# Performance work log

Measured on AMD Instinct MI355X. Metric: run time of the kernel, lower is better.

The kernel has to match this reference:

```python
import jax, jax.numpy as jnp
import numpy as np

B, N, D = 4, 4096, 1024
H, DH = 16, 64  # heads, dim_head; inner_dim = H*DH = 1024
EPS = 1e-6


def setup_inputs() -> dict:
    key = jax.random.key(0)
    ks = jax.random.split(key, 6)
    s = 1.0 / np.sqrt(D)
    return {
        "x": jax.random.normal(ks[0], (B, N, D), dtype=jnp.float32),
        "Wq": jax.random.normal(ks[1], (D, H * DH), dtype=jnp.float32) * s,
        "Wk": jax.random.normal(ks[2], (D, H * DH), dtype=jnp.float32) * s,
        "Wv": jax.random.normal(ks[3], (D, H * DH), dtype=jnp.float32) * s,
        "Wo": jax.random.normal(ks[4], (H * DH, D), dtype=jnp.float32) * s,
        "bo": jnp.zeros((D,), dtype=jnp.float32),
    }


def reference(x, Wq, Wk, Wv, Wo, bo):
    # projections, split heads: b n (h d) -> b h n d
    def split_heads(t):
        b, n, _ = t.shape
        return t.reshape(b, n, H, DH).transpose(0, 2, 1, 3)

    q = split_heads(x @ Wq)
    k = split_heads(x @ Wk)  # context = x (self-attention)
    v = split_heads(x @ Wv)

    # elu feature map: elu(x) + 1
    q = jax.nn.elu(q) + 1.0
    k = jax.nn.elu(k) + 1.0

    # normalizer z[b,h,n,1] = q . sum_n k  + eps
    k_sum = k.sum(axis=2)                                  # b h d
    z = jnp.einsum('bhnd,bhd->bhn', q, k_sum)[..., None] + EPS

    # kv outer-product reduction: O(N d^2)
    kv = jnp.einsum('bhnd,bhne->bhde', k, v)               # b h d e
    out = jnp.einsum('bhnd,bhde->bhne', q, kv) / z         # b h n e

    # merge heads: b h n d -> b n (h d)
    out = out.transpose(0, 2, 1, 3).reshape(x.shape[0], x.shape[1], H * DH)
    return out @ Wo + bo
```

## Files before the change

kernel.cpp:

```cpp
#include <hip/hip_runtime.h>
#include <hip/hip_bf16.h>


#define DEV_INLINE __device__ __forceinline__

typedef short bf16x8 __attribute__((ext_vector_type(8)));
typedef float f32x4  __attribute__((ext_vector_type(4)));

static constexpr int Bb = 4, Nn = 4096, Dd = 1024, Hh = 16, DHd = 64;
static constexpr int Mrows = Bb * Nn;

DEV_INLINE float bf2f(short s) {
  unsigned u = ((unsigned)(unsigned short)s) << 16;
  float f; __builtin_memcpy(&f, &u, 4); return f;
}
DEV_INLINE short f2bf(float f) {
  unsigned u; __builtin_memcpy(&u, &f, 4);
  unsigned r = (u + 0x7fffu + ((u >> 16) & 1u)) >> 16;
  return (short)r;
}

DEV_INLINE void gload16(const void* g, void* l) {
  typedef __attribute__((address_space(1))) const void gv_t;
  typedef __attribute__((address_space(3))) void lv_t;
  __builtin_amdgcn_global_load_lds((gv_t*)g, (lv_t*)l, 16, 0, 0);
}

DEV_INLINE int lds_off(int r_, int c_) {
  return r_ * 128 + ((((c_ >> 3) ^ (r_ & 7)) << 3) | (c_ & 7));
}


__global__ void convert_x_kernel(const float* __restrict__ x, short* __restrict__ xb) {
  const int total = Mrows * 1024 / 4;
  for (int i = blockIdx.x * 256 + threadIdx.x; i < total; i += 2048 * 256) {
    float4 v = ((const float4*)x)[i];
    short4 o;
    o.x = f2bf(v.x); o.y = f2bf(v.y); o.z = f2bf(v.z); o.w = f2bf(v.w);
    ((short4*)xb)[i] = o;
  }
}

__global__ void transposeW_kernel(const float* __restrict__ Wq, const float* __restrict__ Wk,
                                  const float* __restrict__ Wv, const float* __restrict__ Wo,
                                  short* __restrict__ Wt, short* __restrict__ WoT) {
  int z = blockIdx.z;
  const float* W = (z == 0) ? Wq : (z == 1) ? Wk : (z == 2) ? Wv : Wo;
  short* dstb = (z < 3) ? (Wt + (size_t)z * 1024 * 1024) : WoT;
  __shared__ float tile[64][69];
  int t = threadIdx.x;
  int r = t >> 2, c4 = (t & 3) << 4;
  const float* src = W + (blockIdx.y * 64 + r) * 1024 + blockIdx.x * 64 + c4;
  for (int j = 0; j < 4; ++j) {
    float4 v = ((const float4*)src)[j];
    tile[r][c4 + 4 * j + 0] = v.x;
    tile[r][c4 + 4 * j + 1] = v.y;
    tile[r][c4 + 4 * j + 2] = v.z;
    tile[r][c4 + 4 * j + 3] = v.w;
  }
  __syncthreads();
  __attribute__((aligned(16))) short tmp[16];
  for (int j = 0; j < 16; ++j) tmp[j] = f2bf(tile[c4 + j][r]);
  short* dst = dstb + (blockIdx.x * 64 + r) * 1024 + blockIdx.y * 64 + c4;
  ((int4*)dst)[0] = ((int4*)tmp)[0];
  ((int4*)dst)[1] = ((int4*)tmp)[1];
}

template <int MODE>
__global__ __launch_bounds__(256, 2) void gemm128_kernel(
    const short* __restrict__ A, const short* __restrict__ Bt,
    short* __restrict__ q, short* __restrict__ kT, short* __restrict__ vT,
    float* __restrict__ out, const float* __restrict__ bias, int nTilesN) {
  __shared__ __align__(16) short sm[128 * 128];
  short* smA = sm;
  short* smB = sm + 8192;
  const int K = 1024;
  int bid0 = blockIdx.x;
  int xcd = bid0 & 7, local = bid0 >> 3;
  int chunk = local >> 6, rem = local & 63;
  int ncc = nTilesN >> 3;
  int cm = chunk / ncc, cn = chunk % ncc;
  int tm = xcd * 16 + cm * 8 + (rem >> 3);
  int tn = cn * 8 + (rem & 7);

  int t = threadIdx.x, w = t >> 6, lane = t & 63;
  int rl = lane & 15, kg = lane >> 4;
  int wr = w >> 1, wc = w & 1;
  const short* Abase = A + (size_t)tm * 128 * K;
  const short* Bbase = Bt + (size_t)tn * 128 * K;

  f32x4 acc[4][4] = {};
  for (int k0 = 0; k0 < K; k0 += 64) {
    __syncthreads();
    for (int p = 0; p < 4; ++p) {
      int c = p * 256 + t;
      int row = c >> 3, u = c & 7;
      int off = ((u ^ (row & 7)) << 3);
      gload16(Abase + row * K + k0 + off, (char*)smA + p * 4096 + w * 1024);
      gload16(Bbase + row * K + k0 + off, (char*)smB + p * 4096 + w * 1024);
    }
    __syncthreads();
    for (int kk = 0; kk < 2; ++kk) {
      int slot = kk * 4 + kg;
      bf16x8 af[4], bfr[4];
      for (int mt = 0; mt < 4; ++mt) {
        int row = wr * 64 + mt * 16 + rl;
        af[mt] = *(const bf16x8*)&smA[row * 64 + ((slot ^ (row & 7)) << 3)];
      }
      for (int nt = 0; nt < 4; ++nt) {
        int row = wc * 64 + nt * 16 + rl;
        bfr[nt] = *(const bf16x8*)&smB[row * 64 + ((slot ^ (row & 7)) << 3)];
      }
      for (int mt = 0; mt < 4; ++mt)
        for (int nt = 0; nt < 4; ++nt)
          acc[mt][nt] = __builtin_amdgcn_mfma_f32_16x16x32_bf16(af[mt], bfr[nt], acc[mt][nt], 0, 0, 0);
    }
  }
  if (MODE == 1) {
    float* smf = (float*)sm;
    __syncthreads();
    for (int h = 0; h < 2; ++h) {
      if (wr == h) {
        for (int mt = 0; mt < 4; ++mt)
          for (int nt = 0; nt < 4; ++nt)
            for (int r = 0; r < 4; ++r)
              smf[(mt * 16 + kg * 4 + r) * 128 + wc * 64 + nt * 16 + rl] = acc[mt][nt][r];
      }
      __syncthreads();
      for (int i = 0; i < 8; ++i) {
        int idx = i * 256 + t;
        int row = idx >> 5, c4 = (idx & 31) << 2;
        float4 v = *(const float4*)&smf[row * 128 + c4];
        float4 bv = *(const float4*)&bias[tn * 128 + c4];
        v.x += bv.x; v.y += bv.y; v.z += bv.z; v.w += bv.w;
        *(float4*)&out[(size_t)(tm * 128 + h * 64 + row) * Dd + tn * 128 + c4] = v;
      }
      __syncthreads();
    }
    return;
  }
  __syncthreads();
  int sec = tn >> 3;
  int tloc = tn & 7;
  for (int mt = 0; mt < 4; ++mt)
    for (int nt = 0; nt < 4; ++nt)
      for (int r = 0; r < 4; ++r) {
        float v = acc[mt][nt][r];
        if (sec <= 1) v = v > 0.f ? v + 1.f : __expf(v);
        int row = wr * 64 + mt * 16 + kg * 4 + r;
        int col = wc * 64 + nt * 16 + rl;
        int o = (sec == 0) ? lds_off(row, col) : lds_off(col, row);
        sm[o] = f2bf(v);
      }
  __syncthreads();
  if (sec == 0) {
    for (int i = 0; i < 8; ++i) {
      int idx = i * 256 + t;
      int row = idx >> 4, c = idx & 15;
      int col0 = c * 8;
      int gcol = tloc * 128 + col0;
      int h = gcol >> 6, d0 = gcol & 63;
      int grow = tm * 128 + row;
      int b = grow >> 12, n = grow & 4095;
      *(int4*)&q[(((size_t)(b * Hh + h)) * Nn + n) * DHd + d0] = *(const int4*)&sm[lds_off(row, col0)];
    }
  } else {
    short* dst = (sec == 1) ? kT : vT;
    for (int i = 0; i < 8; ++i) {
      int idx = i * 256 + t;
      int dcol = idx >> 4, c = idx & 15;
      int n0 = c * 8;
      int gcol = tloc * 128 + dcol;
      int h = gcol >> 6, d = gcol & 63;
      int grow0 = tm * 128 + n0;
      int b = grow0 >> 12, n = grow0 & 4095;
      *(int4*)&dst[(((size_t)(b * Hh + h)) * DHd + d) * Nn + n] = *(const int4*)&sm[lds_off(dcol, n0)];
    }
  }
}

__global__ void ksum_kernel(const short* __restrict__ kT, float* __restrict__ ksp) {
  int bh = blockIdx.x >> 3, seg = blockIdx.x & 7;
  int t = threadIdx.x;
  int d = t >> 2, sub = t & 3;
  const short* row = kT + ((size_t)bh * DHd + d) * Nn + seg * 512;
  float s = 0.f;
  for (int i = sub * 8; i < 512; i += 32) {
    bf16x8 v = *(const bf16x8*)&row[i];
    for (int j = 0; j < 8; ++j) s += bf2f(v[j]);
  }
  s += __shfl_xor(s, 1);
  s += __shfl_xor(s, 2);
  if (sub == 0) ksp[(bh * 8 + seg) * 64 + d] = s;
}

__global__ __launch_bounds__(256, 2) void kv_kernel(const short* __restrict__ kT,
                                                    const short* __restrict__ vT,
                                                    float* __restrict__ kvp) {
  __shared__ __align__(16) short smK[64 * 128];
  __shared__ __align__(16) short smV[64 * 128];
  int bh = blockIdx.x, seg = blockIdx.y;
  int t = threadIdx.x;
  int w = t >> 6, lane = t & 63, rl = lane & 15, kg = lane >> 4;
  const short* kb = kT + (size_t)bh * DHd * Nn + seg * 1024;
  const short* vb = vT + (size_t)bh * DHd * Nn + seg * 1024;
  f32x4 acc[4] = {};
  for (int n0 = 0; n0 < 1024; n0 += 128) {
    __syncthreads();
    for (int p = 0; p < 4; ++p) {
      int c = p * 256 + t;
      int row = c >> 4, u = c & 15;
      int off = ((u ^ (row & 15)) << 3);
      gload16(kb + row * Nn + n0 + off, (char*)smK + p * 4096 + w * 1024);
      gload16(vb + row * Nn + n0 + off, (char*)smV + p * 4096 + w * 1024);
    }
    __syncthreads();
    for (int kk = 0; kk < 4; ++kk) {
      int slot = kk * 4 + kg;
      int rowA = w * 16 + rl;
      bf16x8 a = *(const bf16x8*)&smK[rowA * 128 + ((slot ^ (rowA & 15)) << 3)];
      for (int nt = 0; nt < 4; ++nt) {
        int rowB = nt * 16 + rl;
        bf16x8 b = *(const bf16x8*)&smV[rowB * 128 + ((slot ^ (rowB & 15)) << 3)];
        acc[nt] = __builtin_amdgcn_mfma_f32_16x16x32_bf16(a, b, acc[nt], 0, 0, 0);
      }
    }
  }
  float* smf = (float*)smK;
  __syncthreads();
  for (int nt = 0; nt < 4; ++nt)
    for (int r = 0; r < 4; ++r)
      smf[(nt * 16 + rl) * 64 + (w * 16 + kg * 4 + r)] = acc[nt][r];
  __syncthreads();
  float* dst = kvp + ((size_t)(bh * 4 + seg)) * 4096;
  for (int i = 0; i < 4; ++i) {
    int idx = i * 256 + t;
    int e = idx >> 4, c4 = (idx & 15) << 2;
    *(float4*)&dst[e * 64 + c4] = *(const float4*)&smf[e * 64 + c4];
  }
}

__global__ void kvc_kernel(const float* __restrict__ kvp, short* __restrict__ kvT) {
  int bh = blockIdx.x, t = threadIdx.x;
  const float* p0 = kvp + (size_t)bh * 4 * 4096;
  for (int rep = 0; rep < 4; ++rep) {
    int idx = rep * 1024 + t * 4;
    float4 a = *(const float4*)&p0[idx];
    float4 b = *(const float4*)&p0[4096 + idx];
    float4 c = *(const float4*)&p0[8192 + idx];
    float4 d = *(const float4*)&p0[12288 + idx];
    short4 o;
    o.x = f2bf(a.x + b.x + c.x + d.x);
    o.y = f2bf(a.y + b.y + c.y + d.y);
    o.z = f2bf(a.z + b.z + c.z + d.z);
    o.w = f2bf(a.w + b.w + c.w + d.w);
    *(short4*)&kvT[(size_t)bh * 4096 + idx] = o;
  }
}

__global__ __launch_bounds__(256, 2) void attn_kernel(const short* __restrict__ q,
                                                      const short* __restrict__ kvT,
                                                      const float* __restrict__ ksp,
                                                      short* __restrict__ attn) {
  int rb = blockIdx.x, bh = blockIdx.y;
  int b = bh >> 4, h = bh & 15;
  __shared__ float sks[64];
  __shared__ __align__(16) short satt[64 * 64];
  int t = threadIdx.x, w = t >> 6, lane = t & 63, rl = lane & 15, kg = lane >> 4;
  if (t < 64) {
    float s = 0.f;
    for (int j = 0; j < 8; ++j) s += ksp[(bh * 8 + j) * 64 + t];
    sks[t] = s;
  }
  __syncthreads();
  int row0 = rb * 64 + w * 16;
  const short* qb = q + ((size_t)bh * Nn + row0) * DHd;
  const short* kvb = kvT + (size_t)bh * 4096;
  f32x4 acc[4] = {};
  float zp = 0.f;
  for (int kk = 0; kk < 2; ++kk) {
    int kb = kk * 32 + kg * 8;
    bf16x8 a = *(const bf16x8*)&qb[rl * DHd + kb];
    for (int j = 0; j < 8; ++j) zp += bf2f(a[j]) * sks[kb + j];
    for (int nt = 0; nt < 4; ++nt) {
      bf16x8 bfr = *(const bf16x8*)&kvb[(nt * 16 + rl) * 64 + kb];
      acc[nt] = __builtin_amdgcn_mfma_f32_16x16x32_bf16(a, bfr, acc[nt], 0, 0, 0);
    }
  }
  zp += __shfl_xor(zp, 16);
  zp += __shfl_xor(zp, 32);
  float zr[4];
  for (int r = 0; r < 4; ++r) zr[r] = __shfl(zp, kg * 4 + r);
  for (int nt = 0; nt < 4; ++nt)
    for (int r = 0; r < 4; ++r)
      satt[(w * 16 + kg * 4 + r) * 64 + nt * 16 + rl] = f2bf(acc[nt][r] / (zr[r] + 1e-6f));
  __syncthreads();
  for (int i = 0; i < 2; ++i) {
    int idx = i * 256 + t;
    int row = idx >> 3, c8 = (idx & 7) << 3;
    int n = rb * 64 + row;
    *(int4*)&attn[((size_t)(b * Nn + n)) * 1024 + h * 64 + c8] = *(const int4*)&satt[row * 64 + c8];
  }
}

extern "C" void kernel_launch(void* const* d_in, const int* in_sizes, int n_in,
                              void* d_out, int out_size, void* d_ws, size_t ws_size,
                              hipStream_t stream) {
  const float* x  = (const float*)d_in[0];
  const float* Wq = (const float*)d_in[1];
  const float* Wk = (const float*)d_in[2];
  const float* Wv = (const float*)d_in[3];
  const float* Wo = (const float*)d_in[4];
  const float* bo = (const float*)d_in[5];
  float* out = (float*)d_out;

  char* ws = (char*)d_ws;
  size_t off = 0;
  auto alloc = [&](size_t bytes) {
    char* p = ws + off;
    off += (bytes + 255) & ~(size_t)255;
    return p;
  };
  short* xb   = (short*)alloc((size_t)Mrows * 1024 * 2);
  short* Wt   = (short*)alloc((size_t)3072 * 1024 * 2);
  short* WoT  = (short*)alloc((size_t)1024 * 1024 * 2);
  short* qb   = (short*)alloc((size_t)64 * Nn * DHd * 2);
  short* kT   = (short*)alloc((size_t)64 * DHd * Nn * 2);
  short* vT   = (short*)alloc((size_t)64 * DHd * Nn * 2);
  float* ksp  = (float*)alloc((size_t)64 * 8 * 64 * 4);
  float* kvp  = (float*)alloc((size_t)64 * 4 * 4096 * 4);
  short* kvT  = (short*)alloc((size_t)64 * 4096 * 2);
  short* attn = (short*)alloc((size_t)Mrows * 1024 * 2);

  convert_x_kernel<<<2048, 256, 0, stream>>>(x, xb);
  transposeW_kernel<<<dim3(16, 16, 4), 256, 0, stream>>>(Wq, Wk, Wv, Wo, Wt, WoT);

  gemm128_kernel<0><<<3072, 256, 0, stream>>>(xb, Wt, qb, kT, vT, nullptr, nullptr, 24);
  ksum_kernel<<<512, 256, 0, stream>>>(kT, ksp);
  kv_kernel<<<dim3(64, 4), 256, 0, stream>>>(kT, vT, kvp);
  kvc_kernel<<<64, 256, 0, stream>>>(kvp, kvT);
  attn_kernel<<<dim3(64, 64), 256, 0, stream>>>(qb, kvT, ksp, attn);
  gemm128_kernel<1><<<1024, 256, 0, stream>>>(attn, WoT, nullptr, nullptr, nullptr, out, bo, 8);
}
```

Before: 239.6 us.

## Replace 128x128 GEMM with 256x256 double-buffered 8-wave pipelined GEMM

```diff
diff --git a/kernel.cpp b/kernel.cpp
--- a/kernel.cpp
+++ b/kernel.cpp
@@ -26,9 +26,8 @@
   __builtin_amdgcn_global_load_lds((gv_t*)g, (lv_t*)l, 16, 0, 0);
 }
 
-DEV_INLINE int lds_off(int r_, int c_) {
-  return r_ * 128 + ((((c_ >> 3) ^ (r_ & 7)) << 3) | (c_ & 7));
-}
+#define SBAR() __builtin_amdgcn_s_barrier()
+#define WAITV(n) asm volatile("s_waitcnt vmcnt(" #n ")" ::: "memory")
 
 
 __global__ void convert_x_kernel(const float* __restrict__ x, short* __restrict__ xb) {
@@ -66,115 +65,178 @@
   ((int4*)dst)[1] = ((int4*)tmp)[1];
 }
 
+
+DEV_INLINE void stage_half(const short* __restrict__ gtile, char* smreg, int h) {
+  int t = threadIdx.x;
+  int lane = t & 63, w = t >> 6;
+#pragma unroll
+  for (int l = 0; l < 2; ++l) {
+    int rbase = h * 128 + l * 64 + w * 8;
+    int row = rbase + (lane >> 3);
+    int slot = lane & 7;
+    gload16(gtile + (size_t)row * 1024 + ((slot ^ (row & 7)) << 3),
+            smreg + (size_t)rbase * 128);
+  }
+}
+
+#define READ_A(set, mbase, kk)                                                     \
+  _Pragma("unroll") for (int m_ = 0; m_ < 4; ++m_) {                               \
+    int row_ = wr * 128 + ((mbase) + m_) * 16 + rl;                                \
+    int slot_ = (kk) * 4 + kg;                                                     \
+    a[m_] = *(const bf16x8*)(smraw + (set) * 65536 + row_ * 128 +                  \
+                             (((slot_ ^ (row_ & 7))) << 4));                       \
+  }
+
+#define READ_B(set, kk)                                                            \
+  _Pragma("unroll") for (int n_ = 0; n_ < 4; ++n_) {                               \
+    int row_ = wc * 64 + n_ * 16 + rl;                                             \
+    int slot_ = (kk) * 4 + kg;                                                     \
+    b[n_] = *(const bf16x8*)(smraw + 32768 + (set) * 65536 + row_ * 128 +          \
+                             (((slot_ ^ (row_ & 7))) << 4));                       \
+  }
+
+#define MF(mbase)                                                                  \
+  __builtin_amdgcn_s_setprio(1);                                                   \
+  _Pragma("unroll") for (int m_ = 0; m_ < 4; ++m_)                                 \
+    _Pragma("unroll") for (int n_ = 0; n_ < 4; ++n_)                               \
+      acc[(mbase) + m_][n_] = __builtin_amdgcn_mfma_f32_16x16x32_bf16(             \
+          a[m_], b[n_], acc[(mbase) + m_][n_], 0, 0, 0);                           \
+  __builtin_amdgcn_s_setprio(0);
+
 template <int MODE>
-__global__ __launch_bounds__(256, 2) void gemm128_kernel(
+__global__ __launch_bounds__(512, 2) void gemm256_kernel(
     const short* __restrict__ A, const short* __restrict__ Bt,
     short* __restrict__ q, short* __restrict__ kT, short* __restrict__ vT,
     float* __restrict__ out, const float* __restrict__ bias, int nTilesN) {
-  __shared__ __align__(16) short sm[128 * 128];
-  short* smA = sm;
-  short* smB = sm + 8192;
-  const int K = 1024;
-  int bid0 = blockIdx.x;
-  int xcd = bid0 & 7, local = bid0 >> 3;
-  int chunk = local >> 6, rem = local & 63;
-  int ncc = nTilesN >> 3;
-  int cm = chunk / ncc, cn = chunk % ncc;
-  int tm = xcd * 16 + cm * 8 + (rem >> 3);
-  int tn = cn * 8 + (rem & 7);
+  __shared__ __align__(16) char smraw[131072];
+  char* smA0 = smraw;
+  char* smB0 = smraw + 32768;
+  char* smA1 = smraw + 65536;
+  char* smB1 = smraw + 98304;
+
+  int bid = blockIdx.x;
+  int xcd = bid & 7, lo = bid >> 3;
+  int tn = lo >> 3, tmg = lo & 7;
+  int tm = xcd * 8 + tmg;
 
   int t = threadIdx.x, w = t >> 6, lane = t & 63;
   int rl = lane & 15, kg = lane >> 4;
-  int wr = w >> 1, wc = w & 1;
-  const short* Abase = A + (size_t)tm * 128 * K;
-  const short* Bbase = Bt + (size_t)tn * 128 * K;
-
-  f32x4 acc[4][4] = {};
-  for (int k0 = 0; k0 < K; k0 += 64) {
-    __syncthreads();
-    for (int p = 0; p < 4; ++p) {
-      int c = p * 256 + t;
-      int row = c >> 3, u = c & 7;
-      int off = ((u ^ (row & 7)) << 3);
-      gload16(Abase + row * K + k0 + off, (char*)smA + p * 4096 + w * 1024);
-      gload16(Bbase + row * K + k0 + off, (char*)smB + p * 4096 + w * 1024);
-    }
-    __syncthreads();
-    for (int kk = 0; kk < 2; ++kk) {
-      int slot = kk * 4 + kg;
-      bf16x8 af[4], bfr[4];
-      for (int mt = 0; mt < 4; ++mt) {
-        int row = wr * 64 + mt * 16 + rl;
-        af[mt] = *(const bf16x8*)&smA[row * 64 + ((slot ^ (row & 7)) << 3)];
+  int wr = w >> 2, wc = w & 3;
+
+  const short* Ab = A + (size_t)tm * 256 * 1024;
+  const short* Bb2 = Bt + (size_t)tn * 256 * 1024;
+
+  f32x4 acc[8][4] = {};
+  bf16x8 a[4], b[4];
+
+  stage_half(Ab, smA0, 0);
+  stage_half(Ab, smA0, 1);
+  stage_half(Bb2, smB0, 0);
+  stage_half(Bb2, smB0, 1);
+  stage_half(Bb2 + 64, smB1, 0);
+  WAITV(2);
+  SBAR();
+
+#pragma unroll 1
+  for (int i = 0; i < 8; ++i) {
+    int k_odd = i * 128 + 64, k_n2 = i * 128 + 128, k_n3 = i * 128 + 192;
+    READ_A(0, 0, 0); READ_B(0, 0);
+    stage_half(Bb2 + k_odd, smB1, 1);
+    SBAR(); MF(0); SBAR();
+    READ_A(0, 4, 0);
+    stage_half(Ab + k_odd, smA1, 0);
+    SBAR(); MF(4); SBAR();
+    READ_A(0, 0, 1); READ_B(0, 1);
+    stage_half(Ab + k_odd, smA1, 1);
+    SBAR(); MF(0); SBAR();
+    READ_A(0, 4, 1);
+    stage_half(Bb2 + k_n2, smB0, 0);
+    WAITV(2); SBAR(); MF(4); SBAR();
+    READ_A(1, 0, 0); READ_B(1, 0);
+    stage_half(Ab + k_n2, smA0, 0);
+    SBAR(); MF(0); SBAR();
+    READ_A(1, 4, 0);
+    stage_half(Ab + k_n2, smA0, 1);
+    SBAR(); MF(4); SBAR();
+    READ_A(1, 0, 1); READ_B(1, 1);
+    stage_half(Bb2 + k_n2, smB0, 1);
+    SBAR(); MF(0); SBAR();
+    READ_A(1, 4, 1);
+    stage_half(Bb2 + k_n3, smB1, 0);
+    WAITV(2); SBAR(); MF(4); SBAR();
+  }
+
+  WAITV(0);
+  SBAR();
+
+  if (MODE == 1) {
+    float* smf = (float*)smraw;
+    for (int hp = 0; hp < 2; ++hp) {
+      if (wr == hp) {
+#pragma unroll
+        for (int m = 0; m < 8; ++m)
+#pragma unroll
+          for (int n = 0; n < 4; ++n)
+#pragma unroll
+            for (int r = 0; r < 4; ++r) {
+              int lrow = m * 16 + kg * 4 + r;
+              int col = wc * 64 + n * 16 + rl;
+              smf[lrow * 256 + ((((col >> 2) ^ (lrow & 7))) << 2) + (col & 3)] = acc[m][n][r];
+            }
       }
-      for (int nt = 0; nt < 4; ++nt) {
-        int row = wc * 64 + nt * 16 + rl;
-        bfr[nt] = *(const bf16x8*)&smB[row * 64 + ((slot ^ (row & 7)) << 3)];
+      SBAR();
+      for (int it = 0; it < 16; ++it) {
+        int idx = it * 512 + t;
+        int row = idx >> 6, c4 = (idx & 63) << 2;
+        float4 v = *(const float4*)&smf[row * 256 + ((((c4 >> 2) ^ (row & 7))) << 2)];
+        float4 bv = *(const float4*)&bias[tn * 256 + c4];
+        v.x += bv.x; v.y += bv.y; v.z += bv.z; v.w += bv.w;
+        *(float4*)&out[(size_t)(tm * 256 + hp * 128 + row) * Dd + tn * 256 + c4] = v;
       }
-      for (int mt = 0; mt < 4; ++mt)
-        for (int nt = 0; nt < 4; ++nt)
-          acc[mt][nt] = __builtin_amdgcn_mfma_f32_16x16x32_bf16(af[mt], bfr[nt], acc[mt][nt], 0, 0, 0);
-    }
-  }
-  if (MODE == 1) {
-    float* smf = (float*)sm;
-    __syncthreads();
-    for (int h = 0; h < 2; ++h) {
-      if (wr == h) {
-        for (int mt = 0; mt < 4; ++mt)
-          for (int nt = 0; nt < 4; ++nt)
-            for (int r = 0; r < 4; ++r)
-              smf[(mt * 16 + kg * 4 + r) * 128 + wc * 64 + nt * 16 + rl] = acc[mt][nt][r];
+      SBAR();
+    }
+    return;
+  }
+
+  short* smc = (short*)smraw;
+  int sec = tn >> 2, tl = tn & 3;
+#pragma unroll
+  for (int m = 0; m < 8; ++m)
+#pragma unroll
+    for (int n = 0; n < 4; ++n)
+#pragma unroll
+      for (int r = 0; r < 4; ++r) {
+        float v = acc[m][n][r];
+        if (sec <= 1) v = v > 0.f ? v + 1.f : __expf(v);
+        int row = wr * 128 + m * 16 + kg * 4 + r;
+        int col = wc * 64 + n * 16 + rl;
+        int rr = (sec == 0) ? row : col;
+        int cc = (sec == 0) ? col : row;
+        smc[rr * 256 + ((((cc >> 3) ^ (rr & 7))) << 3) + (cc & 7)] = f2bf(v);
       }
-      __syncthreads();
-      for (int i = 0; i < 8; ++i) {
-        int idx = i * 256 + t;
-        int row = idx >> 5, c4 = (idx & 31) << 2;
-        float4 v = *(const float4*)&smf[row * 128 + c4];
-        float4 bv = *(const float4*)&bias[tn * 128 + c4];
-        v.x += bv.x; v.y += bv.y; v.z += bv.z; v.w += bv.w;
-        *(float4*)&out[(size_t)(tm * 128 + h * 64 + row) * Dd + tn * 128 + c4] = v;
-      }
-      __syncthreads();
-    }
-    return;
-  }
-  __syncthreads();
-  int sec = tn >> 3;
-  int tloc = tn & 7;
-  for (int mt = 0; mt < 4; ++mt)
-    for (int nt = 0; nt < 4; ++nt)
-      for (int r = 0; r < 4; ++r) {
-        float v = acc[mt][nt][r];
-        if (sec <= 1) v = v > 0.f ? v + 1.f : __expf(v);
-        int row = wr * 64 + mt * 16 + kg * 4 + r;
-        int col = wc * 64 + nt * 16 + rl;
-        int o = (sec == 0) ? lds_off(row, col) : lds_off(col, row);
-        sm[o] = f2bf(v);
-      }
-  __syncthreads();
+  SBAR();
   if (sec == 0) {
-    for (int i = 0; i < 8; ++i) {
-      int idx = i * 256 + t;
-      int row = idx >> 4, c = idx & 15;
-      int col0 = c * 8;
-      int gcol = tloc * 128 + col0;
-      int h = gcol >> 6, d0 = gcol & 63;
-      int grow = tm * 128 + row;
-      int b = grow >> 12, n = grow & 4095;
-      *(int4*)&q[(((size_t)(b * Hh + h)) * Nn + n) * DHd + d0] = *(const int4*)&sm[lds_off(row, col0)];
+    for (int it = 0; it < 16; ++it) {
+      int idx = it * 512 + t;
+      int row = idx >> 5, c8 = (idx & 31) << 3;
+      int4 val = *(const int4*)&smc[row * 256 + ((((c8 >> 3) ^ (row & 7))) << 3)];
+      int grow = tm * 256 + row;
+      int bI = grow >> 12, n = grow & 4095;
+      int g = tl * 256 + c8;
+      int h = g >> 6, d0 = g & 63;
+      *(int4*)&q[(((size_t)(bI * Hh + h)) * Nn + n) * DHd + d0] = val;
     }
   } else {
     short* dst = (sec == 1) ? kT : vT;
-    for (int i = 0; i < 8; ++i) {
-      int idx = i * 256 + t;
-      int dcol = idx >> 4, c = idx & 15;
-      int n0 = c * 8;
-      int gcol = tloc * 128 + dcol;
-      int h = gcol >> 6, d = gcol & 63;
-      int grow0 = tm * 128 + n0;
-      int b = grow0 >> 12, n = grow0 & 4095;
-      *(int4*)&dst[(((size_t)(b * Hh + h)) * DHd + d) * Nn + n] = *(const int4*)&sm[lds_off(dcol, n0)];
+    for (int it = 0; it < 16; ++it) {
+      int idx = it * 512 + t;
+      int dr = idx >> 5, c8 = (idx & 31) << 3;
+      int4 val = *(const int4*)&smc[dr * 256 + ((((c8 >> 3) ^ (dr & 7))) << 3)];
+      int g = tl * 256 + dr;
+      int h = g >> 6, d = g & 63;
+      int grow0 = tm * 256 + c8;
+      int bI = grow0 >> 12, n0 = grow0 & 4095;
+      *(int4*)&dst[(((size_t)(bI * Hh + h)) * DHd + d) * Nn + n0] = val;
     }
   }
 }
@@ -331,14 +393,15 @@
   float* kvp  = (float*)alloc((size_t)64 * 4 * 4096 * 4);
   short* kvT  = (short*)alloc((size_t)64 * 4096 * 2);
   short* attn = (short*)alloc((size_t)Mrows * 1024 * 2);
+  (void)alloc(8192);
 
   convert_x_kernel<<<2048, 256, 0, stream>>>(x, xb);
   transposeW_kernel<<<dim3(16, 16, 4), 256, 0, stream>>>(Wq, Wk, Wv, Wo, Wt, WoT);
 
-  gemm128_kernel<0><<<3072, 256, 0, stream>>>(xb, Wt, qb, kT, vT, nullptr, nullptr, 24);
+  gemm256_kernel<0><<<768, 512, 0, stream>>>(xb, Wt, qb, kT, vT, nullptr, nullptr, 12);
   ksum_kernel<<<512, 256, 0, stream>>>(kT, ksp);
   kv_kernel<<<dim3(64, 4), 256, 0, stream>>>(kT, vT, kvp);
   kvc_kernel<<<64, 256, 0, stream>>>(kvp, kvT);
   attn_kernel<<<dim3(64, 64), 256, 0, stream>>>(qb, kvT, ksp, attn);
-  gemm128_kernel<1><<<1024, 256, 0, stream>>>(attn, WoT, nullptr, nullptr, nullptr, out, bo, 8);
-}
+  gemm256_kernel<1><<<256, 512, 0, stream>>>(attn, WoT, nullptr, nullptr, nullptr, out, bo, 4);
+}
```

Measured after the change: 250.7 us. 4.6% more time.

## Fuse k-sum into projection GEMM epilogue, split kv reduction wider, raise occupancy

Applied to the files above, without the earlier changes.

```diff
diff --git a/kernel.cpp b/kernel.cpp
--- a/kernel.cpp
+++ b/kernel.cpp
@@ -43,12 +43,15 @@
 
 __global__ void transposeW_kernel(const float* __restrict__ Wq, const float* __restrict__ Wk,
                                   const float* __restrict__ Wv, const float* __restrict__ Wo,
-                                  short* __restrict__ Wt, short* __restrict__ WoT) {
+                                  short* __restrict__ Wt, short* __restrict__ WoT,
+                                  float* __restrict__ ksum) {
   int z = blockIdx.z;
+  int t = threadIdx.x;
+  if (z == 0 && blockIdx.y == 0 && blockIdx.x < 16)
+    ksum[blockIdx.x * 256 + t] = 0.f;
   const float* W = (z == 0) ? Wq : (z == 1) ? Wk : (z == 2) ? Wv : Wo;
   short* dstb = (z < 3) ? (Wt + (size_t)z * 1024 * 1024) : WoT;
   __shared__ float tile[64][69];
-  int t = threadIdx.x;
   int r = t >> 2, c4 = (t & 3) << 4;
   const float* src = W + (blockIdx.y * 64 + r) * 1024 + blockIdx.x * 64 + c4;
   for (int j = 0; j < 4; ++j) {
@@ -67,10 +70,11 @@
 }
 
 template <int MODE>
-__global__ __launch_bounds__(256, 2) void gemm128_kernel(
+__global__ __launch_bounds__(256, 4) void gemm128_kernel(
     const short* __restrict__ A, const short* __restrict__ Bt,
     short* __restrict__ q, short* __restrict__ kT, short* __restrict__ vT,
-    float* __restrict__ out, const float* __restrict__ bias, int nTilesN) {
+    float* __restrict__ out, const float* __restrict__ bias,
+    float* __restrict__ ksum, int nTilesN) {
   __shared__ __align__(16) short sm[128 * 128];
   short* smA = sm;
   short* smB = sm + 8192;
@@ -176,22 +180,20 @@
       int b = grow0 >> 12, n = grow0 & 4095;
       *(int4*)&dst[(((size_t)(b * Hh + h)) * DHd + d) * Nn + n] = *(const int4*)&sm[lds_off(dcol, n0)];
     }
-  }
-}
-
-__global__ void ksum_kernel(const short* __restrict__ kT, float* __restrict__ ksp) {
-  int bh = blockIdx.x >> 3, seg = blockIdx.x & 7;
-  int t = threadIdx.x;
-  int d = t >> 2, sub = t & 3;
-  const short* row = kT + ((size_t)bh * DHd + d) * Nn + seg * 512;
-  float s = 0.f;
-  for (int i = sub * 8; i < 512; i += 32) {
-    bf16x8 v = *(const bf16x8*)&row[i];
-    for (int j = 0; j < 8; ++j) s += bf2f(v[j]);
-  }
-  s += __shfl_xor(s, 1);
-  s += __shfl_xor(s, 2);
-  if (sub == 0) ksp[(bh * 8 + seg) * 64 + d] = s;
+    if (sec == 1) {
+      int dcol = t >> 1, half = t & 1;
+      float s = 0.f;
+      for (int c = half * 64; c < half * 64 + 64; ++c)
+        s += bf2f(sm[lds_off(dcol, c)]);
+      s += __shfl_xor(s, 1);
+      if (half == 0) {
+        int g = tloc * 128 + dcol;
+        int h = g >> 6, d = g & 63;
+        int b = (tm * 128) >> 12;
+        atomicAdd(&ksum[(b * Hh + h) * DHd + d], s);
+      }
+    }
+  }
 }
 
 __global__ __launch_bounds__(256, 2) void kv_kernel(const short* __restrict__ kT,
@@ -202,10 +204,10 @@
   int bh = blockIdx.x, seg = blockIdx.y;
   int t = threadIdx.x;
   int w = t >> 6, lane = t & 63, rl = lane & 15, kg = lane >> 4;
-  const short* kb = kT + (size_t)bh * DHd * Nn + seg * 1024;
-  const short* vb = vT + (size_t)bh * DHd * Nn + seg * 1024;
+  const short* kb = kT + (size_t)bh * DHd * Nn + seg * 512;
+  const short* vb = vT + (size_t)bh * DHd * Nn + seg * 512;
   f32x4 acc[4] = {};
-  for (int n0 = 0; n0 < 1024; n0 += 128) {
+  for (int n0 = 0; n0 < 512; n0 += 128) {
     __syncthreads();
     for (int p = 0; p < 4; ++p) {
       int c = p * 256 + t;
@@ -232,7 +234,7 @@
     for (int r = 0; r < 4; ++r)
       smf[(nt * 16 + rl) * 64 + (w * 16 + kg * 4 + r)] = acc[nt][r];
   __syncthreads();
-  float* dst = kvp + ((size_t)(bh * 4 + seg)) * 4096;
+  float* dst = kvp + ((size_t)(bh * 8 + seg)) * 4096;
   for (int i = 0; i < 4; ++i) {
     int idx = i * 256 + t;
     int e = idx >> 4, c4 = (idx & 15) << 2;
@@ -242,36 +244,30 @@
 
 __global__ void kvc_kernel(const float* __restrict__ kvp, short* __restrict__ kvT) {
   int bh = blockIdx.x, t = threadIdx.x;
-  const float* p0 = kvp + (size_t)bh * 4 * 4096;
+  const float* p0 = kvp + (size_t)bh * 8 * 4096;
   for (int rep = 0; rep < 4; ++rep) {
     int idx = rep * 1024 + t * 4;
-    float4 a = *(const float4*)&p0[idx];
-    float4 b = *(const float4*)&p0[4096 + idx];
-    float4 c = *(const float4*)&p0[8192 + idx];
-    float4 d = *(const float4*)&p0[12288 + idx];
+    float4 s = *(const float4*)&p0[idx];
+    for (int j = 1; j < 8; ++j) {
+      float4 a = *(const float4*)&p0[j * 4096 + idx];
+      s.x += a.x; s.y += a.y; s.z += a.z; s.w += a.w;
+    }
     short4 o;
-    o.x = f2bf(a.x + b.x + c.x + d.x);
-    o.y = f2bf(a.y + b.y + c.y + d.y);
-    o.z = f2bf(a.z + b.z + c.z + d.z);
-    o.w = f2bf(a.w + b.w + c.w + d.w);
+    o.x = f2bf(s.x); o.y = f2bf(s.y); o.z = f2bf(s.z); o.w = f2bf(s.w);
     *(short4*)&kvT[(size_t)bh * 4096 + idx] = o;
   }
 }
 
 __global__ __launch_bounds__(256, 2) void attn_kernel(const short* __restrict__ q,
                                                       const short* __restrict__ kvT,
-                                                      const float* __restrict__ ksp,
+                                                      const float* __restrict__ ksum,
                                                       short* __restrict__ attn) {
   int rb = blockIdx.x, bh = blockIdx.y;
   int b = bh >> 4, h = bh & 15;
   __shared__ float sks[64];
   __shared__ __align__(16) short satt[64 * 64];
   int t = threadIdx.x, w = t >> 6, lane = t & 63, rl = lane & 15, kg = lane >> 4;
-  if (t < 64) {
-    float s = 0.f;
-    for (int j = 0; j < 8; ++j) s += ksp[(bh * 8 + j) * 64 + t];
-    sks[t] = s;
-  }
+  if (t < 64) sks[t] = ksum[bh * 64 + t];
   __syncthreads();
   int row0 = rb * 64 + w * 16;
   const short* qb = q + ((size_t)bh * Nn + row0) * DHd;
@@ -327,18 +323,17 @@
   short* qb   = (short*)alloc((size_t)64 * Nn * DHd * 2);
   short* kT   = (short*)alloc((size_t)64 * DHd * Nn * 2);
   short* vT   = (short*)alloc((size_t)64 * DHd * Nn * 2);
-  float* ksp  = (float*)alloc((size_t)64 * 8 * 64 * 4);
-  float* kvp  = (float*)alloc((size_t)64 * 4 * 4096 * 4);
+  float* ksum = (float*)alloc((size_t)64 * 64 * 4);
+  float* kvp  = (float*)alloc((size_t)64 * 8 * 4096 * 4);
   short* kvT  = (short*)alloc((size_t)64 * 4096 * 2);
   short* attn = (short*)alloc((size_t)Mrows * 1024 * 2);
 
   convert_x_kernel<<<2048, 256, 0, stream>>>(x, xb);
-  transposeW_kernel<<<dim3(16, 16, 4), 256, 0, stream>>>(Wq, Wk, Wv, Wo, Wt, WoT);
-
-  gemm128_kernel<0><<<3072, 256, 0, stream>>>(xb, Wt, qb, kT, vT, nullptr, nullptr, 24);
-  ksum_kernel<<<512, 256, 0, stream>>>(kT, ksp);
-  kv_kernel<<<dim3(64, 4), 256, 0, stream>>>(kT, vT, kvp);
+  transposeW_kernel<<<dim3(16, 16, 4), 256, 0, stream>>>(Wq, Wk, Wv, Wo, Wt, WoT, ksum);
+
+  gemm128_kernel<0><<<3072, 256, 0, stream>>>(xb, Wt, qb, kT, vT, nullptr, nullptr, ksum, 24);
+  kv_kernel<<<dim3(64, 8), 256, 0, stream>>>(kT, vT, kvp);
   kvc_kernel<<<64, 256, 0, stream>>>(kvp, kvT);
-  attn_kernel<<<dim3(64, 64), 256, 0, stream>>>(qb, kvT, ksp, attn);
-  gemm128_kernel<1><<<1024, 256, 0, stream>>>(attn, WoT, nullptr, nullptr, nullptr, out, bo, 8);
-}
+  attn_kernel<<<dim3(64, 64), 256, 0, stream>>>(qb, kvT, ksum, attn);
+  gemm128_kernel<1><<<1024, 256, 0, stream>>>(attn, WoT, nullptr, nullptr, nullptr, out, bo, nullptr, 8);
+}
```

New measurement: 235.1 us. About the same (-1.9%).
